# Optimization experiments

Measured on AMD Instinct MI355X. Metric: run time of the kernel, lower is better.

Reference implementation:

```python
import jax, jax.numpy as jnp
import numpy as np

DIM = 256      # in_channels == hidden_channels
INNER = 256    # heads * dim_head
HEADS = 4
DH = 64        # dim_head = hidden_channels // num_heads
EDGE_DIM = 512 # 2 * in_channels
FF = 1024      # 4 * dim ff expansion
DEPTH = 2
OUT = 1
N = 50000      # two stacked graphs of 25000 nodes
E = 100000
HALF = 25000


def setup_inputs() -> dict:
    key = jax.random.key(0)
    ks = iter(jax.random.split(key, 32))

    def lin(fan_in, fan_out):
        w = jax.random.normal(next(ks), (DEPTH, fan_in, fan_out), jnp.float32) * (1.0 / np.sqrt(fan_in))
        b = jnp.zeros((DEPTH, fan_out), jnp.float32)
        return w, b

    x = jax.random.normal(next(ks), (N, DIM), jnp.float32)
    edge_index = jax.random.randint(next(ks), (2, E), 0, HALF, dtype=jnp.int32)
    Wq, bq = lin(DIM, INNER)
    Wkv, bkv = lin(DIM, 2 * INNER)
    We, be = lin(EDGE_DIM, INNER)
    Wo, bo = lin(INNER, DIM)
    W1, b1 = lin(DIM, FF)
    W2, b2 = lin(FF, DIM)
    g_attn = jax.random.normal(next(ks), (DEPTH, 3 * DIM, 1), jnp.float32) * (1.0 / np.sqrt(3 * DIM))
    g_ff = jax.random.normal(next(ks), (DEPTH, 3 * DIM, 1), jnp.float32) * (1.0 / np.sqrt(3 * DIM))
    ln1_g = jnp.ones((DEPTH, DIM), jnp.float32); ln1_b = jnp.zeros((DEPTH, DIM), jnp.float32)
    ln2_g = jnp.ones((DEPTH, DIM), jnp.float32); ln2_b = jnp.zeros((DEPTH, DIM), jnp.float32)
    Wout = jax.random.normal(next(ks), (DIM, OUT), jnp.float32) * (1.0 / np.sqrt(DIM))
    bout = jnp.zeros((OUT,), jnp.float32)
    return dict(x=x, edge_index=edge_index, ln1_g=ln1_g, ln1_b=ln1_b, Wq=Wq, bq=bq,
                Wkv=Wkv, bkv=bkv, We=We, be=be, Wo=Wo, bo=bo, g_attn=g_attn,
                ln2_g=ln2_g, ln2_b=ln2_b, W1=W1, b1=b1, W2=W2, b2=b2, g_ff=g_ff,
                Wout=Wout, bout=bout)


def _layer_norm(x, g, b):
    mu = jnp.mean(x, axis=-1, keepdims=True)
    var = jnp.mean(jnp.square(x - mu), axis=-1, keepdims=True)
    return (x - mu) * jax.lax.rsqrt(var + 1e-5) * g + b


def _gated_residual(x, res, w):
    # gate = sigmoid(Linear_no_bias(cat(x, res, x - res)))
    gate = jax.nn.sigmoid(jnp.concatenate([x, res, x - res], axis=-1) @ w)  # [n,1]
    return x * gate + res * (1.0 - gate)


def _forward(x, edge_index, ln1_g, ln1_b, Wq, bq, Wkv, bkv, We, be, Wo, bo, g_attn,
             ln2_g, ln2_b, W1, b1, W2, b2, g_ff, Wout, bout):
    src, dst = edge_index[0], edge_index[1]
    # edge_attr = cat(x[src], x[dst]) as built in DeepGraphTransformer_mse.forward
    edge_attr = jnp.concatenate([x[src], x[dst]], axis=-1)  # [E, 2*DIM]
    nodes = x
    n = nodes.shape[0]
    scale = DH ** -0.5
    for l in range(DEPTH):
        xn = _layer_norm(nodes, ln1_g[l], ln1_b[l])
        q = xn @ Wq[l] + bq[l]                                   # [n, INNER]
        k, v = jnp.split(xn @ Wkv[l] + bkv[l], 2, axis=-1)       # [n, INNER] each
        e = edge_attr @ We[l] + be[l]                            # [E, INNER]
        qe = q[dst].reshape(-1, HEADS, DH)                       # [E,H,Dh]
        ke = (k[src] + e).reshape(-1, HEADS, DH)
        ve = (v[src] + e).reshape(-1, HEADS, DH)
        sim = jnp.einsum('ehd,ehd->eh', qe, ke) * scale          # [E,H]
        smax = jax.ops.segment_max(sim, dst, num_segments=n)     # [n,H] (-inf for empty)
        ez = jnp.exp(sim - smax[dst])
        denom = jax.ops.segment_sum(ez, dst, num_segments=n)
        attn = ez / denom[dst]                                   # softmax over incoming edges
        agg = jax.ops.segment_sum(attn[:, :, None] * ve, dst, num_segments=n)
        attn_out = agg.reshape(n, INNER) @ Wo[l] + bo[l]         # [n, DIM]
        nodes = _gated_residual(attn_out, nodes, g_attn[l])
        xn2 = _layer_norm(nodes, ln2_g[l], ln2_b[l])
        h = jax.nn.gelu(xn2 @ W1[l] + b1[l], approximate=False) @ W2[l] + b2[l]
        nodes = _gated_residual(h, nodes, g_ff[l])
    z = nodes @ Wout + bout                                      # [n, OUT]
    return z


def reference(x, edge_index, ln1_g, ln1_b, Wq, bq, Wkv, bkv, We, be, Wo, bo, g_attn,
              ln2_g, ln2_b, W1, b1, W2, b2, g_ff, Wout, bout):
    z = _forward(x, edge_index, ln1_g, ln1_b, Wq, bq, Wkv, bkv, We, be, Wo, bo, g_attn,
                 ln2_g, ln2_b, W1, b1, W2, b2, g_ff, Wout, bout)
    half = z.shape[0] // 2
    z_old, z_new = z[:half], z[half:]
    return (z_new.reshape(-1), z_old, z_new)
```

## Files before the change

### kernel.cpp

```cpp
#include <hip/hip_runtime.h>
#include <cmath>

#define N_NODES 50000
#define N_EDGES 100000
#define HALF_N  25000
#define DIM     256
#define NDEPTH  2
#define MAXDEG  64

#define WT_QKVE 0
#define WT_WO   524288
#define WT_W1   589824
#define WT_W2   851968
#define WT_LAYER 1114112

typedef __bf16 bf16;
typedef bf16 bf16x8 __attribute__((ext_vector_type(8)));
typedef bf16 bf16x4 __attribute__((ext_vector_type(4)));
typedef float f32x4 __attribute__((ext_vector_type(4)));

__device__ __forceinline__ void lds_barrier() {
  asm volatile("s_waitcnt lgkmcnt(0)" ::: "memory");
  __builtin_amdgcn_s_barrier();
  __builtin_amdgcn_sched_barrier(0);
}

__device__ __forceinline__ float wave_sum(float v) {
  v += __shfl_xor(v, 1);
  v += __shfl_xor(v, 2);
  v += __shfl_xor(v, 4);
  v += __shfl_xor(v, 8);
  v += __shfl_xor(v, 16);
  v += __shfl_xor(v, 32);
  return v;
}

__device__ __forceinline__ float fast_gelu(float v) {
  float ax = fabsf(v) * 0.70710678118654752f;
  float t = __builtin_amdgcn_rcpf(fmaf(0.3275911f, ax, 1.0f));
  float p = t * fmaf(t, fmaf(t, fmaf(t, fmaf(t, 1.061405429f, -1.453152027f),
                                     1.421413741f), -0.284496736f), 0.254829592f);
  float e = __expf(-ax * ax);
  float erfv = fmaf(-p, e, 1.0f);
  float ph = copysignf(erfv, v);
  return 0.5f * v * (1.0f + ph);
}

__global__ void ln0_kernel(const float* __restrict__ in, const float* __restrict__ g,
                           const float* __restrict__ b, bf16* __restrict__ A2) {
  int row = blockIdx.x * 4 + (threadIdx.x >> 6);
  if (row >= HALF_N) return;
  int lane = threadIdx.x & 63;
  float4 x = reinterpret_cast<const float4*>(in + (size_t)row * DIM)[lane];
  float mu = wave_sum(x.x + x.y + x.z + x.w) * (1.0f / DIM);
  float d0 = x.x - mu, d1 = x.y - mu, d2 = x.z - mu, d3 = x.w - mu;
  float var = wave_sum(d0*d0 + d1*d1 + d2*d2 + d3*d3) * (1.0f / DIM);
  float r = rsqrtf(var + 1e-5f);
  float4 gv = reinterpret_cast<const float4*>(g)[lane];
  float4 bv = reinterpret_cast<const float4*>(b)[lane];
  bf16x4 o;
  o[0] = (bf16)(d0 * r * gv.x + bv.x);
  o[1] = (bf16)(d1 * r * gv.y + bv.y);
  o[2] = (bf16)(d2 * r * gv.z + bv.z);
  o[3] = (bf16)(d3 * r * gv.w + bv.w);
  *reinterpret_cast<bf16x4*>(A2 + (size_t)row * 512 + lane * 4) = o;
}

template<int KK, int NJ>
__global__ __launch_bounds__(256, 2) void gemm_nloop(
    const bf16* __restrict__ A, const bf16* __restrict__ Wp,
    const float* __restrict__ bias, bf16* __restrict__ C, int M) {
  constexpr int STEPS = KK / 64;
  __shared__ bf16x8 As[KK * 8];
  __shared__ bf16 Cs[64 * 128];
  const int tid = threadIdx.x;
  const int lane = tid & 63, wv = tid >> 6;
  const int wr = wv >> 1, wc = wv & 1;
  const int lm = lane & 15, kb = (lane >> 4) & 3;
  const int row0 = blockIdx.x * 64;
#pragma unroll
  for (int i = 0; i < KK / 32; ++i) {
    int idx = tid + i * 256;
    int row = idx & 63, k8 = idx >> 6;
    int rga = row0 + row; if (rga >= M) rga = M - 1;
    As[idx] = *reinterpret_cast<const bf16x8*>(A + (size_t)rga * KK + k8 * 8);
  }
  lds_barrier();
  const bf16x8* wb = reinterpret_cast<const bf16x8*>(Wp) + kb * 128 + wc * 64 + lm;
  for (int jn = 0; jn < NJ; ++jn) {
    f32x4 acc[2][4] = {};
    for (int st = 0; st < STEPS; ++st) {
#pragma unroll
      for (int ks = 0; ks < 2; ++ks) {
        bf16x8 bfr[4], af[2];
#pragma unroll
        for (int ni = 0; ni < 4; ++ni)
          bfr[ni] = wb[(size_t)jn * (KK * 16) + st * 1024 + ks * 512 + ni * 16];
#pragma unroll
        for (int mi = 0; mi < 2; ++mi)
          af[mi] = As[(st * 8 + ks * 4 + kb) * 64 + wr * 32 + mi * 16 + lm];
#pragma unroll
        for (int mi = 0; mi < 2; ++mi)
#pragma unroll
          for (int ni = 0; ni < 4; ++ni)
            acc[mi][ni] = __builtin_amdgcn_mfma_f32_16x16x32_bf16(af[mi], bfr[ni], acc[mi][ni], 0, 0, 0);
      }
    }
    lds_barrier();
#pragma unroll
    for (int ni = 0; ni < 4; ++ni) {
      int c = wc * 64 + ni * 16 + lm;
      float bval = bias[jn * 128 + c];
#pragma unroll
      for (int mi = 0; mi < 2; ++mi)
#pragma unroll
        for (int e = 0; e < 4; ++e) {
          int r = wr * 32 + mi * 16 + kb * 4 + e;
          Cs[r * 128 + c] = (bf16)(acc[mi][ni][e] + bval);
        }
    }
    lds_barrier();
    bf16x8* C8 = reinterpret_cast<bf16x8*>(C);
    const bf16x8* Cs8 = (const bf16x8*)Cs;
#pragma unroll
    for (int i = 0; i < 4; ++i) {
      int idx = tid + i * 256;
      int row = idx >> 4, c8 = idx & 15;
      int grow = row0 + row;
      if (grow < M) C8[(size_t)grow * (NJ * 16) + jn * 16 + c8] = Cs8[row * 16 + c8];
    }
  }
}

__global__ __launch_bounds__(256, 2) void wo_fused(
    const bf16* __restrict__ A, const bf16* __restrict__ Wp,
    const float* __restrict__ bo, const float* __restrict__ gattn,
    const float* __restrict__ ln2g, const float* __restrict__ ln2b,
    float* __restrict__ nodes, bf16* __restrict__ xn, int M) {
  __shared__ bf16x8 As[2048];
  __shared__ bf16 Cs[64 * 256];
  const int tid = threadIdx.x;
  const int lane = tid & 63, wv = tid >> 6;
  const int wr = wv >> 1, wc = wv & 1;
  const int lm = lane & 15, kb = (lane >> 4) & 3;
  const int row0 = blockIdx.x * 64;
#pragma unroll
  for (int i = 0; i < 8; ++i) {
    int idx = tid + i * 256;
    int row = idx & 63, k8 = idx >> 6;
    int rga = row0 + row; if (rga >= M) rga = M - 1;
    As[idx] = *reinterpret_cast<const bf16x8*>(A + (size_t)rga * 256 + k8 * 8);
  }
  lds_barrier();
  const bf16x8* wb = reinterpret_cast<const bf16x8*>(Wp) + kb * 128 + wc * 64 + lm;
  for (int jn = 0; jn < 2; ++jn) {
    f32x4 acc[2][4] = {};
#pragma unroll
    for (int st = 0; st < 4; ++st) {
#pragma unroll
      for (int ks = 0; ks < 2; ++ks) {
        bf16x8 bfr[4], af[2];
#pragma unroll
        for (int ni = 0; ni < 4; ++ni)
          bfr[ni] = wb[jn * 4096 + st * 1024 + ks * 512 + ni * 16];
#pragma unroll
        for (int mi = 0; mi < 2; ++mi)
          af[mi] = As[(st * 8 + ks * 4 + kb) * 64 + wr * 32 + mi * 16 + lm];
#pragma unroll
        for (int mi = 0; mi < 2; ++mi)
#pragma unroll
          for (int ni = 0; ni < 4; ++ni)
            acc[mi][ni] = __builtin_amdgcn_mfma_f32_16x16x32_bf16(af[mi], bfr[ni], acc[mi][ni], 0, 0, 0);
      }
    }
#pragma unroll
    for (int ni = 0; ni < 4; ++ni) {
      int cfull = jn * 128 + wc * 64 + ni * 16 + lm;
      float bval = bo[cfull];
#pragma unroll
      for (int mi = 0; mi < 2; ++mi)
#pragma unroll
        for (int e = 0; e < 4; ++e) {
          int r = wr * 32 + mi * 16 + kb * 4 + e;
          int ch = (cfull >> 3) ^ (r & 7);
          Cs[r * 256 + ch * 8 + (cfull & 7)] = (bf16)(acc[mi][ni][e] + bval);
        }
    }
  }
  lds_barrier();
  for (int pass = 0; pass < 16; ++pass) {
    int r = pass * 4 + wv;
    int grow = row0 + r;
    if (grow >= M) continue;
    int ch = (lane >> 1) ^ (r & 7);
    bf16x4 c4 = *reinterpret_cast<const bf16x4*>(Cs + r * 256 + ch * 8 + (lane & 1) * 4);
    float x0 = (float)c4[0], x1 = (float)c4[1], x2 = (float)c4[2], x3 = (float)c4[3];
    float4 rv = reinterpret_cast<const float4*>(nodes + (size_t)grow * 256)[lane];
    float4 w0 = reinterpret_cast<const float4*>(gattn)[lane];
    float4 w1 = reinterpret_cast<const float4*>(gattn + 256)[lane];
    float4 w2 = reinterpret_cast<const float4*>(gattn + 512)[lane];
    float dot = x0 * (w0.x + w2.x) + rv.x * (w1.x - w2.x)
              + x1 * (w0.y + w2.y) + rv.y * (w1.y - w2.y)
              + x2 * (w0.z + w2.z) + rv.z * (w1.z - w2.z)
              + x3 * (w0.w + w2.w) + rv.w * (w1.w - w2.w);
    dot = wave_sum(dot);
    float gate = 1.0f / (1.0f + __expf(-dot));
    float n0 = fmaf(x0 - rv.x, gate, rv.x);
    float n1 = fmaf(x1 - rv.y, gate, rv.y);
    float n2 = fmaf(x2 - rv.z, gate, rv.z);
    float n3 = fmaf(x3 - rv.w, gate, rv.w);
    float4 o; o.x = n0; o.y = n1; o.z = n2; o.w = n3;
    reinterpret_cast<float4*>(nodes + (size_t)grow * 256)[lane] = o;
    float mu = wave_sum(n0 + n1 + n2 + n3) * (1.0f / DIM);
    float d0 = n0 - mu, d1 = n1 - mu, d2 = n2 - mu, d3 = n3 - mu;
    float var = wave_sum(d0*d0 + d1*d1 + d2*d2 + d3*d3) * (1.0f / DIM);
    float rs = rsqrtf(var + 1e-5f);
    float4 gv = reinterpret_cast<const float4*>(ln2g)[lane];
    float4 bv = reinterpret_cast<const float4*>(ln2b)[lane];
    bf16x4 ob;
    ob[0] = (bf16)(d0 * rs * gv.x + bv.x);
    ob[1] = (bf16)(d1 * rs * gv.y + bv.y);
    ob[2] = (bf16)(d2 * rs * gv.z + bv.z);
    ob[3] = (bf16)(d3 * rs * gv.w + bv.w);
    *reinterpret_cast<bf16x4*>(xn + (size_t)grow * 256 + lane * 4) = ob;
  }
}

template<int LAST>
__global__ __launch_bounds__(512, 4) void ff_fused(
    const bf16* __restrict__ A, const bf16* __restrict__ W1p,
    const float* __restrict__ b1, const bf16* __restrict__ W2p,
    const float* __restrict__ b2, float* __restrict__ nodes,
    const float* __restrict__ gff, const float* __restrict__ ln1g,
    const float* __restrict__ ln1b, bf16* __restrict__ A2,
    const float* __restrict__ Wout, const float* __restrict__ bout,
    float* __restrict__ out, int M) {
  __shared__ char smem[49152];
  bf16x8* Xs = (bf16x8*)smem;
  bf16*   Cs = (bf16*)smem;
  bf16x8* Hs = (bf16x8*)(smem + 32768);
  const int tid = threadIdx.x;
  const int lane = tid & 63, wv = tid >> 6;
  const int wr = wv >> 2, wc = wv & 3;
  const int lm = lane & 15, kb = (lane >> 4) & 3;
  const int row0 = blockIdx.x * 64;
#pragma unroll
  for (int i = 0; i < 4; ++i) {
    int idx = tid + i * 512;
    int row = idx & 63, k8 = idx >> 6;
    int rga = row0 + row; if (rga >= M) rga = M - 1;
    Xs[idx] = *reinterpret_cast<const bf16x8*>(A + (size_t)rga * 256 + k8 * 8);
  }
  lds_barrier();
  const bf16x8* w1b = (const bf16x8*)W1p + kb * 128 + wc * 32 + lm;
  const bf16x8* w2b = (const bf16x8*)W2p + kb * 256 + wc * 64 + lm;
  f32x4 acc[2][4] = {};
  bf16* hsb = (bf16*)Hs;
  for (int j = 0; j < 8; ++j) {
    bf16x8 pf2[8];
#pragma unroll
    for (int ks = 0; ks < 2; ++ks)
#pragma unroll
      for (int ni = 0; ni < 4; ++ni)
        pf2[ks * 4 + ni] = w2b[j * 4096 + ks * 1024 + ni * 16];
    f32x4 acc1[2][2] = {};
#pragma unroll
    for (int half = 0; half < 2; ++half) {
#pragma unroll
      for (int ks = 0; ks < 4; ++ks) {
        bf16x8 bfr[2], af[2];
#pragma unroll
        for (int ni = 0; ni < 2; ++ni)
          bfr[ni] = w1b[j * 4096 + half * 2048 + ks * 512 + ni * 16];
#pragma unroll
        for (int mi = 0; mi < 2; ++mi)
          af[mi] = Xs[(half * 16 + ks * 4 + kb) * 64 + wr * 32 + mi * 16 + lm];
#pragma unroll
        for (int mi = 0; mi < 2; ++mi)
#pragma unroll
          for (int ni = 0; ni < 2; ++ni)
            acc1[mi][ni] = __builtin_amdgcn_mfma_f32_16x16x32_bf16(af[mi], bfr[ni], acc1[mi][ni], 0, 0, 0);
      }
    }
    lds_barrier();
#pragma unroll
    for (int ni = 0; ni < 2; ++ni) {
      int c = wc * 32 + ni * 16 + lm;
      float bval = b1[j * 128 + c];
#pragma unroll
      for (int mi = 0; mi < 2; ++mi)
#pragma unroll
        for (int e = 0; e < 4; ++e) {
          int r = wr * 32 + mi * 16 + kb * 4 + e;
          float v = fast_gelu(acc1[mi][ni][e] + bval);
          hsb[((c >> 3) * 64 + r) * 8 + (c & 7)] = (bf16)v;
        }
    }
    lds_barrier();
#pragma unroll
    for (int h2 = 0; h2 < 2; ++h2) {
#pragma unroll
      for (int ks = 0; ks < 2; ++ks) {
        bf16x8 bfr[4], af[2];
#pragma unroll
        for (int ni = 0; ni < 4; ++ni)
          bfr[ni] = (h2 == 0) ? pf2[ks * 4 + ni]
                              : w2b[j * 4096 + 2048 + ks * 1024 + ni * 16];
#pragma unroll
        for (int mi = 0; mi < 2; ++mi)
          af[mi] = Hs[(h2 * 8 + ks * 4 + kb) * 64 + wr * 32 + mi * 16 + lm];
#pragma unroll
        for (int mi = 0; mi < 2; ++mi)
#pragma unroll
          for (int ni = 0; ni < 4; ++ni)
            acc[mi][ni] = __builtin_amdgcn_mfma_f32_16x16x32_bf16(af[mi], bfr[ni], acc[mi][ni], 0, 0, 0);
      }
    }
  }
#pragma unroll
  for (int ni = 0; ni < 4; ++ni) {
    int c = wc * 64 + ni * 16 + lm;
    float bval = b2[c];
#pragma unroll
    for (int mi = 0; mi < 2; ++mi)
#pragma unroll
      for (int e = 0; e < 4; ++e) {
        int r = wr * 32 + mi * 16 + kb * 4 + e;
        int ch = (c >> 3) ^ (r & 7);
        Cs[r * 256 + ch * 8 + (c & 7)] = (bf16)(acc[mi][ni][e] + bval);
      }
  }
  lds_barrier();
  for (int pass = 0; pass < 8; ++pass) {
    int r = pass * 8 + wv;
    int grow = row0 + r;
    if (grow >= M) continue;
    int ch = (lane >> 1) ^ (r & 7);
    bf16x4 c4 = *reinterpret_cast<const bf16x4*>(Cs + r * 256 + ch * 8 + (lane & 1) * 4);
    float x0 = (float)c4[0], x1 = (float)c4[1], x2 = (float)c4[2], x3 = (float)c4[3];
    float4 rv = reinterpret_cast<const float4*>(nodes + (size_t)grow * 256)[lane];
    float4 w0 = reinterpret_cast<const float4*>(gff)[lane];
    float4 w1 = reinterpret_cast<const float4*>(gff + 256)[lane];
    float4 w2 = reinterpret_cast<const float4*>(gff + 512)[lane];
    float dot = x0 * (w0.x + w2.x) + rv.x * (w1.x - w2.x)
              + x1 * (w0.y + w2.y) + rv.y * (w1.y - w2.y)
              + x2 * (w0.z + w2.z) + rv.z * (w1.z - w2.z)
              + x3 * (w0.w + w2.w) + rv.w * (w1.w - w2.w);
    dot = wave_sum(dot);
    float gate = 1.0f / (1.0f + __expf(-dot));
    float n0 = fmaf(x0 - rv.x, gate, rv.x);
    float n1 = fmaf(x1 - rv.y, gate, rv.y);
    float n2 = fmaf(x2 - rv.z, gate, rv.z);
    float n3 = fmaf(x3 - rv.w, gate, rv.w);
    if (LAST) {
      float4 wo4 = reinterpret_cast<const float4*>(Wout)[lane];
      float z = n0 * wo4.x + n1 * wo4.y + n2 * wo4.z + n3 * wo4.w;
      z = wave_sum(z);
      if (lane == 0) {
        z += bout[0];
        if (grow < HALF_N) {
          out[HALF_N + grow] = z;
        } else {
          int jj = grow - HALF_N;
          out[jj] = z;
          out[2 * HALF_N + jj] = z;
        }
      }
    } else {
      float4 o; o.x = n0; o.y = n1; o.z = n2; o.w = n3;
      reinterpret_cast<float4*>(nodes + (size_t)grow * 256)[lane] = o;
      if (grow < HALF_N) {
        float mu = wave_sum(n0 + n1 + n2 + n3) * (1.0f / DIM);
        float d0 = n0 - mu, d1 = n1 - mu, d2 = n2 - mu, d3 = n3 - mu;
        float var = wave_sum(d0*d0 + d1*d1 + d2*d2 + d3*d3) * (1.0f / DIM);
        float rs = rsqrtf(var + 1e-5f);
        float4 gv = reinterpret_cast<const float4*>(ln1g)[lane];
        float4 bv = reinterpret_cast<const float4*>(ln1b)[lane];
        bf16x4 ob;
        ob[0] = (bf16)(d0 * rs * gv.x + bv.x);
        ob[1] = (bf16)(d1 * rs * gv.y + bv.y);
        ob[2] = (bf16)(d2 * rs * gv.z + bv.z);
        ob[3] = (bf16)(d3 * rs * gv.w + bv.w);
        *reinterpret_cast<bf16x4*>(A2 + (size_t)grow * 512 + lane * 4) = ob;
      }
    }
  }
}

__global__ void ell_build(const int* __restrict__ ei, int* __restrict__ deg,
                          int* __restrict__ ell) {
  int e = blockIdx.x * 256 + threadIdx.x;
  if (e >= N_EDGES) return;
  int s = ei[e], d = ei[N_EDGES + e];
  int pos = atomicAdd(&deg[d], 1);
  if (pos < MAXDEG) ell[d * MAXDEG + pos] = s;
}

__global__ void attn_gather(const int* __restrict__ deg, const int* __restrict__ ell,
                            const bf16* __restrict__ qkv, bf16* __restrict__ agg) {
  int d = blockIdx.x * 4 + (threadIdx.x >> 6);
  if (d >= HALF_N) return;
  int lane = threadIdx.x & 63;
  int cnt = deg[d]; if (cnt > MAXDEG) cnt = MAXDEG;
  const bf16* qr = qkv + (size_t)d * 1024;
  bf16x4 qb = *reinterpret_cast<const bf16x4*>(qr + lane * 4);
  float q0 = (float)qb[0], q1 = (float)qb[1], q2 = (float)qb[2], q3 = (float)qb[3];
  float m = -INFINITY, den = 0.0f, a0 = 0.0f, a1 = 0.0f, a2 = 0.0f, a3 = 0.0f;
  for (int i = 0; i < cnt; ++i) {
    int s = ell[d * MAXDEG + i];
    bf16x8 kv8 = *reinterpret_cast<const bf16x8*>(qkv + (size_t)s * 1024 + 256 + lane * 8);
    float p = q0 * (float)kv8[0] + q1 * (float)kv8[1] +
              q2 * (float)kv8[2] + q3 * (float)kv8[3];
    p += __shfl_xor(p, 1); p += __shfl_xor(p, 2);
    p += __shfl_xor(p, 4); p += __shfl_xor(p, 8);
    float sim = p * 0.125f;
    float nm = fmaxf(m, sim);
    float sc = __expf(m - nm);
    float w  = __expf(sim - nm);
    den = den * sc + w;
    a0 = a0 * sc + w * (float)kv8[4];
    a1 = a1 * sc + w * (float)kv8[5];
    a2 = a2 * sc + w * (float)kv8[6];
    a3 = a3 * sc + w * (float)kv8[7];
    m = nm;
  }
  bf16x4 o;
  if (cnt > 0) {
    float inv = 1.0f / den;
    bf16x4 eb = *reinterpret_cast<const bf16x4*>(qr + 768 + lane * 4);
    o[0] = (bf16)(a0 * inv + (float)eb[0]);
    o[1] = (bf16)(a1 * inv + (float)eb[1]);
    o[2] = (bf16)(a2 * inv + (float)eb[2]);
    o[3] = (bf16)(a3 * inv + (float)eb[3]);
  } else {
    o[0] = (bf16)0.0f; o[1] = (bf16)0.0f; o[2] = (bf16)0.0f; o[3] = (bf16)0.0f;
  }
  *reinterpret_cast<bf16x4*>(agg + (size_t)d * DIM + lane * 4) = o;
}

template<int DO_LN>
__global__ void gr_ln(const float* __restrict__ fb,
                      float* __restrict__ nodes, const float* __restrict__ w,
                      const float* __restrict__ g, const float* __restrict__ b,
                      bf16* __restrict__ xn, int rows) {
  int r = blockIdx.x * 4 + (threadIdx.x >> 6);
  if (r >= rows) return;
  int lane = threadIdx.x & 63;
  float4 f = reinterpret_cast<const float4*>(fb)[lane];
  float x0 = f.x, x1 = f.y, x2 = f.z, x3 = f.w;
  float4 rv = reinterpret_cast<const float4*>(nodes + (size_t)r * DIM)[lane];
  float4 w0 = reinterpret_cast<const float4*>(w)[lane];
  float4 w1 = reinterpret_cast<const float4*>(w + 256)[lane];
  float4 w2 = reinterpret_cast<const float4*>(w + 512)[lane];
  float p = x0 * (w0.x + w2.x) + rv.x * (w1.x - w2.x)
          + x1 * (w0.y + w2.y) + rv.y * (w1.y - w2.y)
          + x2 * (w0.z + w2.z) + rv.z * (w1.z - w2.z)
          + x3 * (w0.w + w2.w) + rv.w * (w1.w - w2.w);
  p = wave_sum(p);
  float gate = 1.0f / (1.0f + __expf(-p));
  float n0 = x0 * gate + rv.x * (1.0f - gate);
  float n1 = x1 * gate + rv.y * (1.0f - gate);
  float n2 = x2 * gate + rv.z * (1.0f - gate);
  float n3 = x3 * gate + rv.w * (1.0f - gate);
  float4 o; o.x = n0; o.y = n1; o.z = n2; o.w = n3;
  reinterpret_cast<float4*>(nodes + (size_t)r * DIM)[lane] = o;
  if (DO_LN) {
    float mu = wave_sum(n0 + n1 + n2 + n3) * (1.0f / DIM);
    float d0 = n0 - mu, d1 = n1 - mu, d2 = n2 - mu, d3 = n3 - mu;
    float var = wave_sum(d0*d0 + d1*d1 + d2*d2 + d3*d3) * (1.0f / DIM);
    float rs = rsqrtf(var + 1e-5f);
    float4 gv = reinterpret_cast<const float4*>(g)[lane];
    float4 bv = reinterpret_cast<const float4*>(b)[lane];
    bf16x4 ob;
    ob[0] = (bf16)(d0 * rs * gv.x + bv.x);
    ob[1] = (bf16)(d1 * rs * gv.y + bv.y);
    ob[2] = (bf16)(d2 * rs * gv.z + bv.z);
    ob[3] = (bf16)(d3 * rs * gv.w + bv.w);
    *reinterpret_cast<bf16x4*>(xn + (size_t)r * DIM + lane * 4) = ob;
  }
}

__global__ void prep_w(const float* __restrict__ Wq, const float* __restrict__ Wkv,
                       const float* __restrict__ We, const float* __restrict__ Wo,
                       const float* __restrict__ W1, const float* __restrict__ W2,
                       bf16* __restrict__ wt) {
  int idx = blockIdx.x * 256 + threadIdx.x;
  if (idx >= 2 * WT_LAYER) return;
  int l = idx / WT_LAYER, r = idx % WT_LAYER;
  float v;
  if (r < 524288) {
    int jn = r >> 16, t = r & 65535;
    int k8 = t >> 10, u = t & 1023, n = u >> 3, e = u & 7;
    int ncol = jn * 128 + n, k = k8 * 8 + e;
    if (ncol < 256) {
      v = (k < 256) ? Wq[l * 65536 + k * 256 + ncol] : 0.0f;
    } else if (ncol < 768) {
      int u2 = ncol - 256;
      int c = (u2 >> 3) * 4 + (u2 & 3);
      int half = (u2 >> 2) & 1;
      if (k < 256) v = Wkv[l * 131072 + k * 512 + half * 256 + c];
      else         v = We[l * 131072 + (k - 256) * 256 + c];
    } else {
      int c = ncol - 768;
      v = (k < 256) ? 0.0f : We[l * 131072 + k * 256 + c];
    }
  } else if (r < 589824) {
    int rr = r - 524288;
    int jn = rr >> 15, t = rr & 32767;
    int k8 = t >> 10, u = t & 1023, n = u >> 3, e = u & 7;
    v = Wo[l * 65536 + (k8 * 8 + e) * 256 + jn * 128 + n];
  } else if (r < 851968) {
    int rr = r - 589824;
    int j = rr >> 15, t = rr & 32767;
    int k8 = t >> 10, u = t & 1023, n = u >> 3, e = u & 7;
    v = W1[l * 262144 + (k8 * 8 + e) * 1024 + j * 128 + n];
  } else {
    int rr = r - 851968;
    int j = rr >> 15, t = rr & 32767;
    int k8 = t >> 11, u = t & 2047, n = u >> 3, e = u & 7;
    v = W2[l * 262144 + (j * 128 + k8 * 8 + e) * 256 + n];
  }
  wt[idx] = (bf16)v;
}

__global__ void prep_bias(const float* __restrict__ bq, const float* __restrict__ bkv,
                          const float* __restrict__ be, float* __restrict__ biasq) {
  int i = blockIdx.x * 256 + threadIdx.x;
  if (i >= 2048) return;
  int l = i >> 10, n = i & 1023;
  float v;
  if (n < 256) v = bq[l * 256 + n];
  else if (n < 768) {
    int u2 = n - 256;
    int c = (u2 >> 3) * 4 + (u2 & 3);
    int half = (u2 >> 2) & 1;
    v = bkv[l * 512 + half * 256 + c];
  } else v = be[l * 256 + (n - 768)];
  biasq[i] = v;
}

__global__ void prep_x(const float* __restrict__ x, bf16* __restrict__ A2) {
  int i = blockIdx.x * 256 + threadIdx.x;
  if (i >= HALF_N * 64) return;
  int row = i >> 6, c = i & 63;
  float4 v = reinterpret_cast<const float4*>(x)[i];
  bf16x4 o;
  o[0] = (bf16)v.x; o[1] = (bf16)v.y; o[2] = (bf16)v.z; o[3] = (bf16)v.w;
  *reinterpret_cast<bf16x4*>(A2 + (size_t)row * 512 + 256 + c * 4) = o;
}

extern "C" void kernel_launch(void* const* d_in, const int* in_sizes, int n_in,
                              void* d_out, int out_size, void* d_ws, size_t ws_size,
                              hipStream_t stream) {
  const float* x     = (const float*)d_in[0];
  const int*   ei    = (const int*)d_in[1];
  const float* ln1_g = (const float*)d_in[2];
  const float* ln1_b = (const float*)d_in[3];
  const float* Wq    = (const float*)d_in[4];
  const float* bq    = (const float*)d_in[5];
  const float* Wkv   = (const float*)d_in[6];
  const float* bkv   = (const float*)d_in[7];
  const float* We    = (const float*)d_in[8];
  const float* be    = (const float*)d_in[9];
  const float* Wo    = (const float*)d_in[10];
  const float* bo    = (const float*)d_in[11];
  const float* g_attn= (const float*)d_in[12];
  const float* ln2_g = (const float*)d_in[13];
  const float* ln2_b = (const float*)d_in[14];
  const float* W1    = (const float*)d_in[15];
  const float* b1    = (const float*)d_in[16];
  const float* W2    = (const float*)d_in[17];
  const float* b2    = (const float*)d_in[18];
  const float* g_ff  = (const float*)d_in[19];
  const float* Wout  = (const float*)d_in[20];
  const float* bout  = (const float*)d_in[21];
  float* out = (float*)d_out;

  char* base = (char*)d_ws;
  float* nodes   = (float*)base;  base += (size_t)N_NODES * DIM * 4;
  bf16*  A2      = (bf16*)base;   base += (size_t)HALF_N * 512 * 2;
  bf16*  xn_bf   = (bf16*)base;   base += (size_t)N_NODES * DIM * 2;
  bf16*  qkv     = (bf16*)base;   base += (size_t)HALF_N * 1024 * 2;
  bf16*  agg     = (bf16*)base;   base += (size_t)HALF_N * DIM * 2;
  bf16*  wt      = (bf16*)base;   base += (size_t)2 * WT_LAYER * 2;
  float* biasq   = (float*)base;  base += 2048 * 4;
  int*   deg     = (int*)base;    base += HALF_N * 4;
  int*   ell     = (int*)base;    base += (size_t)HALF_N * MAXDEG * 4;

  hipMemcpyAsync(nodes, x, (size_t)N_NODES * DIM * sizeof(float),
                 hipMemcpyDeviceToDevice, stream);
  prep_w<<<(2 * WT_LAYER + 255) / 256, 256, 0, stream>>>(Wq, Wkv, We, Wo, W1, W2, wt);
  prep_bias<<<8, 256, 0, stream>>>(bq, bkv, be, biasq);
  prep_x<<<(HALF_N * 64 + 255) / 256, 256, 0, stream>>>(x, A2);
  hipMemsetAsync(deg, 0, HALF_N * sizeof(int), stream);
  ell_build<<<(N_EDGES + 255) / 256, 256, 0, stream>>>(ei, deg, ell);

  const int GP_H = (HALF_N + 63) / 64;
  const int GP_N = (N_NODES + 63) / 64;

  for (int l = 0; l < NDEPTH; ++l) {
    const bf16* wl = wt + (size_t)l * WT_LAYER;
    if (l == 0)
      ln0_kernel<<<(HALF_N + 3) / 4, 256, 0, stream>>>(x, ln1_g, ln1_b, A2);
    gemm_nloop<512, 8><<<GP_H, 256, 0, stream>>>(A2, wl + WT_QKVE, biasq + l * 1024, qkv, HALF_N);
    attn_gather<<<(HALF_N + 3) / 4, 256, 0, stream>>>(deg, ell, qkv, agg);
    wo_fused<<<GP_H, 256, 0, stream>>>(agg, wl + WT_WO, bo + l * DIM,
                                       g_attn + l * 768, ln2_g + l * DIM, ln2_b + l * DIM,
                                       nodes, xn_bf, HALF_N);
    gr_ln<1><<<(HALF_N + 3) / 4, 256, 0, stream>>>(
        bo + l * DIM, nodes + (size_t)HALF_N * DIM, g_attn + l * 768,
        ln2_g + l * DIM, ln2_b + l * DIM, xn_bf + (size_t)HALF_N * DIM, HALF_N);
    if (l < NDEPTH - 1) {
      ff_fused<0><<<GP_N, 512, 0, stream>>>(
          xn_bf, wl + WT_W1, b1 + l * 1024, wl + WT_W2, b2 + l * DIM,
          nodes, g_ff + l * 768, ln1_g + (l + 1) * DIM, ln1_b + (l + 1) * DIM, A2,
          nullptr, nullptr, nullptr, N_NODES);
    } else {
      ff_fused<1><<<GP_N, 512, 0, stream>>>(
          xn_bf, wl + WT_W1, b1 + l * 1024, wl + WT_W2, b2 + l * DIM,
          nodes, g_ff + l * 768, nullptr, nullptr, nullptr,
          Wout, bout, out, N_NODES);
    }
  }
}
```

Baseline: 508.5 us.

## Stream FF weights into LDS via async DMA, prefetch GEMM weights, unroll attention gather

The fused feed-forward kernel now stages W1/W2 tiles through a triple-buffered LDS ring filled with global_load_lds, using vmcnt-based phase syncs and s_setprio around the MFMA blocks. This hides weight-load latency behind compute. In exchange, LDS grows to 144KB and occupancy drops to one block per CU. Separately, the generic GEMM prefetches the first weight fragment of each output tile, and the attention gather processes two edges per iteration to expose more memory-level parallelism.

```diff
diff --git a/kernel.cpp b/kernel.cpp
--- a/kernel.cpp
+++ b/kernel.cpp
@@ -21,6 +21,16 @@
 
 __device__ __forceinline__ void lds_barrier() {
   asm volatile("s_waitcnt lgkmcnt(0)" ::: "memory");
+  __builtin_amdgcn_s_barrier();
+  __builtin_amdgcn_sched_barrier(0);
+}
+__device__ __forceinline__ void phase_sync4() {
+  asm volatile("s_waitcnt vmcnt(4) lgkmcnt(0)" ::: "memory");
+  __builtin_amdgcn_s_barrier();
+  __builtin_amdgcn_sched_barrier(0);
+}
+__device__ __forceinline__ void phase_sync0() {
+  asm volatile("s_waitcnt vmcnt(0) lgkmcnt(0)" ::: "memory");
   __builtin_amdgcn_s_barrier();
   __builtin_amdgcn_sched_barrier(0);
 }
@@ -85,17 +95,26 @@
     int rga = row0 + row; if (rga >= M) rga = M - 1;
     As[idx] = *reinterpret_cast<const bf16x8*>(A + (size_t)rga * KK + k8 * 8);
   }
+  const bf16x8* wb = reinterpret_cast<const bf16x8*>(Wp) + kb * 128 + wc * 64 + lm;
+  bf16x8 pfr[4];
+#pragma unroll
+  for (int ni = 0; ni < 4; ++ni) pfr[ni] = wb[ni * 16];
   lds_barrier();
-  const bf16x8* wb = reinterpret_cast<const bf16x8*>(Wp) + kb * 128 + wc * 64 + lm;
   for (int jn = 0; jn < NJ; ++jn) {
     f32x4 acc[2][4] = {};
+#pragma unroll
     for (int st = 0; st < STEPS; ++st) {
 #pragma unroll
       for (int ks = 0; ks < 2; ++ks) {
         bf16x8 bfr[4], af[2];
-#pragma unroll
-        for (int ni = 0; ni < 4; ++ni)
-          bfr[ni] = wb[(size_t)jn * (KK * 16) + st * 1024 + ks * 512 + ni * 16];
+        if (st == 0 && ks == 0) {
+#pragma unroll
+          for (int ni = 0; ni < 4; ++ni) bfr[ni] = pfr[ni];
+        } else {
+#pragma unroll
+          for (int ni = 0; ni < 4; ++ni)
+            bfr[ni] = wb[(size_t)jn * (KK * 16) + st * 1024 + ks * 512 + ni * 16];
+        }
 #pragma unroll
         for (int mi = 0; mi < 2; ++mi)
           af[mi] = As[(st * 8 + ks * 4 + kb) * 64 + wr * 32 + mi * 16 + lm];
@@ -105,6 +124,11 @@
           for (int ni = 0; ni < 4; ++ni)
             acc[mi][ni] = __builtin_amdgcn_mfma_f32_16x16x32_bf16(af[mi], bfr[ni], acc[mi][ni], 0, 0, 0);
       }
+    }
+    if (jn + 1 < NJ) {
+#pragma unroll
+      for (int ni = 0; ni < 4; ++ni)
+        pfr[ni] = wb[(size_t)(jn + 1) * (KK * 16) + ni * 16];
     }
     lds_barrier();
 #pragma unroll
@@ -227,7 +251,7 @@
 }
 
 template<int LAST>
-__global__ __launch_bounds__(512, 4) void ff_fused(
+__global__ __launch_bounds__(512, 1) void ff_fused(
     const bf16* __restrict__ A, const bf16* __restrict__ W1p,
     const float* __restrict__ b1, const bf16* __restrict__ W2p,
     const float* __restrict__ b2, float* __restrict__ nodes,
@@ -235,15 +259,19 @@
     const float* __restrict__ ln1b, bf16* __restrict__ A2,
     const float* __restrict__ Wout, const float* __restrict__ bout,
     float* __restrict__ out, int M) {
-  __shared__ char smem[49152];
+  __shared__ char smem[147456];
   bf16x8* Xs = (bf16x8*)smem;
   bf16*   Cs = (bf16*)smem;
   bf16x8* Hs = (bf16x8*)(smem + 32768);
+  bf16x8* WB = (bf16x8*)(smem + 49152);
   const int tid = threadIdx.x;
   const int lane = tid & 63, wv = tid >> 6;
   const int wr = wv >> 2, wc = wv & 3;
   const int lm = lane & 15, kb = (lane >> 4) & 3;
   const int row0 = blockIdx.x * 64;
+  const bf16x8* W1p8 = (const bf16x8*)W1p;
+  const bf16x8* W2p8 = (const bf16x8*)W2p;
+
 #pragma unroll
   for (int i = 0; i < 4; ++i) {
     int idx = tid + i * 512;
@@ -251,38 +279,71 @@
     int rga = row0 + row; if (rga >= M) rga = M - 1;
     Xs[idx] = *reinterpret_cast<const bf16x8*>(A + (size_t)rga * 256 + k8 * 8);
   }
-  lds_barrier();
-  const bf16x8* w1b = (const bf16x8*)W1p + kb * 128 + wc * 32 + lm;
-  const bf16x8* w2b = (const bf16x8*)W2p + kb * 256 + wc * 64 + lm;
+
+  auto dma = [&](int p) {
+    if (p >= 32) return;
+    const bf16x8* srcb = ((p & 2) ? W2p8 : W1p8)
+                         + ((p >> 2) * 4096 + (p & 1) * 2048) + tid;
+    bf16x8* dstb = WB + (p % 3) * 2048 + tid;
+#pragma unroll
+    for (int i = 0; i < 4; ++i)
+      __builtin_amdgcn_global_load_lds(
+          (const __attribute__((address_space(1))) unsigned int*)(srcb + i * 512),
+          (__attribute__((address_space(3))) unsigned int*)(dstb + i * 512),
+          16, 0, 0);
+  };
+  dma(0);
+  dma(1);
+
   f32x4 acc[2][4] = {};
   bf16* hsb = (bf16*)Hs;
   for (int j = 0; j < 8; ++j) {
-    bf16x8 pf2[8];
-#pragma unroll
-    for (int ks = 0; ks < 2; ++ks)
-#pragma unroll
-      for (int ni = 0; ni < 4; ++ni)
-        pf2[ks * 4 + ni] = w2b[j * 4096 + ks * 1024 + ni * 16];
+    int p = j * 4;
     f32x4 acc1[2][2] = {};
-#pragma unroll
-    for (int half = 0; half < 2; ++half) {
+    phase_sync4();
+    dma(p + 2);
+    {
+      const bf16x8* B = WB + (j % 3) * 2048;
+      __builtin_amdgcn_s_setprio(1);
 #pragma unroll
       for (int ks = 0; ks < 4; ++ks) {
         bf16x8 bfr[2], af[2];
 #pragma unroll
         for (int ni = 0; ni < 2; ++ni)
-          bfr[ni] = w1b[j * 4096 + half * 2048 + ks * 512 + ni * 16];
-#pragma unroll
-        for (int mi = 0; mi < 2; ++mi)
-          af[mi] = Xs[(half * 16 + ks * 4 + kb) * 64 + wr * 32 + mi * 16 + lm];
+          bfr[ni] = B[ks * 512 + kb * 128 + wc * 32 + ni * 16 + lm];
+#pragma unroll
+        for (int mi = 0; mi < 2; ++mi)
+          af[mi] = Xs[(ks * 4 + kb) * 64 + wr * 32 + mi * 16 + lm];
 #pragma unroll
         for (int mi = 0; mi < 2; ++mi)
 #pragma unroll
           for (int ni = 0; ni < 2; ++ni)
             acc1[mi][ni] = __builtin_amdgcn_mfma_f32_16x16x32_bf16(af[mi], bfr[ni], acc1[mi][ni], 0, 0, 0);
       }
-    }
-    lds_barrier();
+      __builtin_amdgcn_s_setprio(0);
+    }
+    phase_sync4();
+    dma(p + 3);
+    {
+      const bf16x8* B = WB + ((j + 1) % 3) * 2048;
+      __builtin_amdgcn_s_setprio(1);
+#pragma unroll
+      for (int ks = 0; ks < 4; ++ks) {
+        bf16x8 bfr[2], af[2];
+#pragma unroll
+        for (int ni = 0; ni < 2; ++ni)
+          bfr[ni] = B[ks * 512 + kb * 128 + wc * 32 + ni * 16 + lm];
+#pragma unroll
+        for (int mi = 0; mi < 2; ++mi)
+          af[mi] = Xs[(16 + ks * 4 + kb) * 64 + wr * 32 + mi * 16 + lm];
+#pragma unroll
+        for (int mi = 0; mi < 2; ++mi)
+#pragma unroll
+          for (int ni = 0; ni < 2; ++ni)
+            acc1[mi][ni] = __builtin_amdgcn_mfma_f32_16x16x32_bf16(af[mi], bfr[ni], acc1[mi][ni], 0, 0, 0);
+      }
+      __builtin_amdgcn_s_setprio(0);
+    }
 #pragma unroll
     for (int ni = 0; ni < 2; ++ni) {
       int c = wc * 32 + ni * 16 + lm;
@@ -296,25 +357,49 @@
           hsb[((c >> 3) * 64 + r) * 8 + (c & 7)] = (bf16)v;
         }
     }
-    lds_barrier();
-#pragma unroll
-    for (int h2 = 0; h2 < 2; ++h2) {
+    phase_sync4();
+    dma(p + 4);
+    {
+      const bf16x8* B = WB + ((j + 2) % 3) * 2048;
+      __builtin_amdgcn_s_setprio(1);
 #pragma unroll
       for (int ks = 0; ks < 2; ++ks) {
         bf16x8 bfr[4], af[2];
 #pragma unroll
         for (int ni = 0; ni < 4; ++ni)
-          bfr[ni] = (h2 == 0) ? pf2[ks * 4 + ni]
-                              : w2b[j * 4096 + 2048 + ks * 1024 + ni * 16];
-#pragma unroll
-        for (int mi = 0; mi < 2; ++mi)
-          af[mi] = Hs[(h2 * 8 + ks * 4 + kb) * 64 + wr * 32 + mi * 16 + lm];
+          bfr[ni] = B[ks * 1024 + kb * 256 + wc * 64 + ni * 16 + lm];
+#pragma unroll
+        for (int mi = 0; mi < 2; ++mi)
+          af[mi] = Hs[(ks * 4 + kb) * 64 + wr * 32 + mi * 16 + lm];
 #pragma unroll
         for (int mi = 0; mi < 2; ++mi)
 #pragma unroll
           for (int ni = 0; ni < 4; ++ni)
             acc[mi][ni] = __builtin_amdgcn_mfma_f32_16x16x32_bf16(af[mi], bfr[ni], acc[mi][ni], 0, 0, 0);
       }
+      __builtin_amdgcn_s_setprio(0);
+    }
+    if (j == 7) phase_sync0(); else phase_sync4();
+    dma(p + 5);
+    {
+      const bf16x8* B = WB + (j % 3) * 2048;
+      __builtin_amdgcn_s_setprio(1);
+#pragma unroll
+      for (int ks = 0; ks < 2; ++ks) {
+        bf16x8 bfr[4], af[2];
+#pragma unroll
+        for (int ni = 0; ni < 4; ++ni)
+          bfr[ni] = B[ks * 1024 + kb * 256 + wc * 64 + ni * 16 + lm];
+#pragma unroll
+        for (int mi = 0; mi < 2; ++mi)
+          af[mi] = Hs[(8 + ks * 4 + kb) * 64 + wr * 32 + mi * 16 + lm];
+#pragma unroll
+        for (int mi = 0; mi < 2; ++mi)
+#pragma unroll
+          for (int ni = 0; ni < 4; ++ni)
+            acc[mi][ni] = __builtin_amdgcn_mfma_f32_16x16x32_bf16(af[mi], bfr[ni], acc[mi][ni], 0, 0, 0);
+      }
+      __builtin_amdgcn_s_setprio(0);
     }
   }
 #pragma unroll
@@ -406,17 +491,39 @@
   bf16x4 qb = *reinterpret_cast<const bf16x4*>(qr + lane * 4);
   float q0 = (float)qb[0], q1 = (float)qb[1], q2 = (float)qb[2], q3 = (float)qb[3];
   float m = -INFINITY, den = 0.0f, a0 = 0.0f, a1 = 0.0f, a2 = 0.0f, a3 = 0.0f;
-  for (int i = 0; i < cnt; ++i) {
+  int i = 0;
+  for (; i + 2 <= cnt; i += 2) {
+    int s0 = ell[d * MAXDEG + i];
+    int s1 = ell[d * MAXDEG + i + 1];
+    bf16x8 k0 = *reinterpret_cast<const bf16x8*>(qkv + (size_t)s0 * 1024 + 256 + lane * 8);
+    bf16x8 k1 = *reinterpret_cast<const bf16x8*>(qkv + (size_t)s1 * 1024 + 256 + lane * 8);
+    float p0 = q0 * (float)k0[0] + q1 * (float)k0[1] + q2 * (float)k0[2] + q3 * (float)k0[3];
+    float p1 = q0 * (float)k1[0] + q1 * (float)k1[1] + q2 * (float)k1[2] + q3 * (float)k1[3];
+    p0 += __shfl_xor(p0, 1); p1 += __shfl_xor(p1, 1);
+    p0 += __shfl_xor(p0, 2); p1 += __shfl_xor(p1, 2);
+    p0 += __shfl_xor(p0, 4); p1 += __shfl_xor(p1, 4);
+    p0 += __shfl_xor(p0, 8); p1 += __shfl_xor(p1, 8);
+    float s0v = p0 * 0.125f, s1v = p1 * 0.125f;
+    float nm = fmaxf(m, fmaxf(s0v, s1v));
+    float sc = __expf(m - nm);
+    float w0 = __expf(s0v - nm), w1 = __expf(s1v - nm);
+    den = den * sc + w0 + w1;
+    a0 = a0 * sc + w0 * (float)k0[4] + w1 * (float)k1[4];
+    a1 = a1 * sc + w0 * (float)k0[5] + w1 * (float)k1[5];
+    a2 = a2 * sc + w0 * (float)k0[6] + w1 * (float)k1[6];
+    a3 = a3 * sc + w0 * (float)k0[7] + w1 * (float)k1[7];
+    m = nm;
+  }
+  if (i < cnt) {
     int s = ell[d * MAXDEG + i];
     bf16x8 kv8 = *reinterpret_cast<const bf16x8*>(qkv + (size_t)s * 1024 + 256 + lane * 8);
-    float p = q0 * (float)kv8[0] + q1 * (float)kv8[1] +
-              q2 * (float)kv8[2] + q3 * (float)kv8[3];
+    float p = q0 * (float)kv8[0] + q1 * (float)kv8[1] + q2 * (float)kv8[2] + q3 * (float)kv8[3];
     p += __shfl_xor(p, 1); p += __shfl_xor(p, 2);
     p += __shfl_xor(p, 4); p += __shfl_xor(p, 8);
     float sim = p * 0.125f;
     float nm = fmaxf(m, sim);
     float sc = __expf(m - nm);
-    float w  = __expf(sim - nm);
+    float w = __expf(sim - nm);
     den = den * sc + w;
     a0 = a0 * sc + w * (float)kv8[4];
     a1 = a1 * sc + w * (float)kv8[5];
```

Result: slower. 579.9 us (+14.0%).
